# Kernel tuning notes

Measured on AMD Instinct MI355X. Metric: run time of the kernel, lower is better.

## Reference

```python
import jax, jax.numpy as jnp
import numpy as np

B, T, C, H = 4, 2048, 1024, 16
D = C // H  # head dim 64


def setup_inputs() -> dict:
    key = jax.random.key(0)
    ks = jax.random.split(key, 5)
    s = 1.0 / np.sqrt(C)
    return {
        "x": jax.random.normal(ks[0], (B, T, C), jnp.float32),
        "Wq": jax.random.normal(ks[1], (C, C), jnp.float32) * s,
        "bq": jnp.zeros((C,), jnp.float32),
        "Wk": jax.random.normal(ks[2], (C, C), jnp.float32) * s,
        "bk": jnp.zeros((C,), jnp.float32),
        "Wv": jax.random.normal(ks[3], (C, C), jnp.float32) * s,
        "bv": jnp.zeros((C,), jnp.float32),
        "Wp": jax.random.normal(ks[4], (C, C), jnp.float32) * s,
        "bp": jnp.zeros((C,), jnp.float32),
    }


def reference(x, Wq, bq, Wk, bk, Wv, bv, Wp, bp):
    # project and split heads: [B,T,C] -> [B,H,T,D]
    def heads(w, b):
        return (x @ w.T + b).reshape(B, T, H, D).transpose(0, 2, 1, 3)

    q = heads(Wq, bq)
    k = heads(Wk, bk)
    v = heads(Wv, bv)

    att = jnp.einsum("bhqd,bhkd->bhqk", q, k) * (1.0 / np.sqrt(D))
    causal = jnp.tril(jnp.ones((T, T), bool))  # [T,T]
    att = jnp.where(causal[None, None], att, -jnp.inf)
    att = jax.nn.softmax(att, axis=-1)
    # dropout prob is 0.0 -> identity
    y = jnp.einsum("bhqk,bhkd->bhqd", att, v)
    y = y.transpose(0, 2, 1, 3).reshape(B, T, C)
    return y @ Wp.T + bp
```

## Files before the change

### kernel.cpp

```cpp
#include <hip/hip_runtime.h>
#include <hip/hip_bf16.h>

#define BB 4
#define TT 2048
#define CC 1024
#define HH 16
#define DD 64
#define PSTR 72

typedef unsigned short u16;
typedef __attribute__((ext_vector_type(8))) short bf16x8;
typedef __attribute__((ext_vector_type(4))) float f32x4;
typedef __attribute__((ext_vector_type(16))) float f32x16;

__device__ __forceinline__ float bf2f(u16 v) {
    union { unsigned u; float f; } c; c.u = ((unsigned)v) << 16; return c.f;
}
__device__ __forceinline__ u16 f2bf(float f) {
    union { float f; unsigned u; } c; c.f = f;
    unsigned u = c.u + 0x7fffu + ((c.u >> 16) & 1u);
    return (u16)(u >> 16);
}
__device__ __forceinline__ float fast_exp2(float x) {
    float r;
    asm volatile("v_exp_f32 %0, %1\n\ts_nop 1" : "=v"(r) : "v"(x));
    return r;
}
__device__ __forceinline__ unsigned pack_bf16(unsigned b0, unsigned b1) {
    unsigned d;
    asm("v_perm_b32 %0, %1, %2, %3" : "=v"(d) : "v"(b1), "v"(b0), "v"(0x07060302u));
    return d;
}
__device__ __forceinline__ uint2 pack4(float v0, float v1, float v2, float v3) {
    uint2 pk;
    pk.x = pack_bf16(__float_as_uint(v0) + 0x8000u, __float_as_uint(v1) + 0x8000u);
    pk.y = pack_bf16(__float_as_uint(v2) + 0x8000u, __float_as_uint(v3) + 0x8000u);
    return pk;
}
__device__ __forceinline__ unsigned cvtpk_bf16(float lo, float hi) {
    unsigned r;
    asm("v_cvt_pk_bf16_f32 %0, %1, %2" : "=v"(r) : "v"(lo), "v"(hi));
    return r;
}
__device__ __forceinline__ void gload16(const u16* g, u16* l) {
    __builtin_amdgcn_global_load_lds(
        (const __attribute__((address_space(1))) void*)g,
        (__attribute__((address_space(3))) void*)l, 16, 0, 0);
}

__device__ __forceinline__ int detect_bf16(const u16* __restrict__ xprobe, int* sh) {
    const int t = threadIdx.x;
    u16 hh = xprobe[2 * t];
    int e = (hh >> 7) & 0xFF;
    unsigned long long m = __ballot(e >= 118 && e <= 132);
    if ((t & 63) == 0) sh[t >> 6] = __popcll(m);
    __syncthreads();
    return (sh[0] + sh[1] + sh[2] + sh[3]) >= 128;
}

struct CastArgs {
    const void* src[9];
    u16* dst[9];
    int blk_start[10];
    int n[9];
};
__global__ __launch_bounds__(256) void cast_all(CastArgs a, const u16* __restrict__ xprobe) {
    __shared__ int sh[4];
    const int isbf = detect_bf16(xprobe, sh);
    int b = blockIdx.x;
    int s = 0;
    while (s < 8 && b >= a.blk_start[s + 1]) s++;
    int i0 = (b - a.blk_start[s]) * 2048 + threadIdx.x * 8;
    if (i0 + 8 > a.n[s]) return;
    if (isbf) {
        *(uint4*)&a.dst[s][i0] = *(const uint4*)&((const u16*)a.src[s])[i0];
    } else {
        const float* sp = (const float*)a.src[s];
        u16 tmp[8];
#pragma unroll
        for (int j = 0; j < 8; j++) tmp[j] = f2bf(sp[i0 + j]);
        *(uint4*)&a.dst[s][i0] = *(uint4*)tmp;
    }
}

__device__ __forceinline__ void gemm_core(
    const u16* __restrict__ X, const u16* __restrict__ W,
    u16* Als, u16* Bls, f32x16 (&acc)[2][2],
    int m0, int n0, int wave, int lane, int wm, int wn)
{
    const int l32 = lane & 31;
    const int hv  = lane >> 5;
    int srow[4], sch[4];
#pragma unroll
    for (int c = 0; c < 4; c++) {
        srow[c] = wave * 32 + c * 8 + (lane >> 3);
        sch[c]  = (lane & 7) ^ (srow[c] & 7);
    }

    for (int k0 = 0; k0 < CC; k0 += 64) {
        __syncthreads();
#pragma unroll
        for (int c = 0; c < 4; c++) {
            gload16(&X[(size_t)(m0 + srow[c]) * CC + k0 + sch[c] * 8],
                    &Als[wave * 2048 + c * 512]);
            gload16(&W[(size_t)(n0 + srow[c]) * CC + k0 + sch[c] * 8],
                    &Bls[wave * 2048 + c * 512]);
        }
        __syncthreads();

#pragma unroll
        for (int ks = 0; ks < 4; ks++) {
            const int sw = ((ks * 2 + hv) ^ (l32 & 7)) * 8;
            bf16x8 a[2], b[2];
#pragma unroll
            for (int i = 0; i < 2; i++)
                a[i] = *(const bf16x8*)&Als[(wm + i * 32 + l32) * 64 + sw];
#pragma unroll
            for (int j = 0; j < 2; j++)
                b[j] = *(const bf16x8*)&Bls[(wn + j * 32 + l32) * 64 + sw];
#pragma unroll
            for (int i = 0; i < 2; i++)
#pragma unroll
                for (int j = 0; j < 2; j++)
                    acc[i][j] = __builtin_amdgcn_mfma_f32_32x32x16_bf16(
                        b[j], a[i], acc[i][j], 0, 0, 0);
        }
    }
}

__global__ __launch_bounds__(256, 2) void gemm_qkv(
    const u16* __restrict__ X,
    const u16* __restrict__ Wq, const u16* __restrict__ Wk, const u16* __restrict__ Wv,
    const u16* __restrict__ bq, const u16* __restrict__ bk, const u16* __restrict__ bv,
    u16* __restrict__ Q, u16* __restrict__ K, u16* __restrict__ VT)
{
    __shared__ __align__(16) u16 Als[128 * 64];
    __shared__ __align__(16) u16 Bls[3 * 128 * 64];

    const int tid  = threadIdx.x;
    const int wave = tid >> 6;
    const int lane = tid & 63;
    const int l32  = lane & 31;
    const int hv   = lane >> 5;
    const int m0   = blockIdx.x * 128;
    const int n0   = blockIdx.y * 128;
    const int wm   = (wave >> 1) * 64;
    const int wn   = (wave & 1) * 64;

    const u16* Ws[3]  = {Wq, Wk, Wv};

    f32x16 acc[3][2][2];
#pragma unroll
    for (int z = 0; z < 3; z++)
#pragma unroll
        for (int i = 0; i < 2; i++)
#pragma unroll
            for (int j = 0; j < 2; j++) acc[z][i][j] = (f32x16)0.0f;

    int srow[4], sch[4];
#pragma unroll
    for (int c = 0; c < 4; c++) {
        srow[c] = wave * 32 + c * 8 + (lane >> 3);
        sch[c]  = (lane & 7) ^ (srow[c] & 7);
    }

    for (int k0 = 0; k0 < CC; k0 += 64) {
        __syncthreads();
#pragma unroll
        for (int c = 0; c < 4; c++)
            gload16(&X[(size_t)(m0 + srow[c]) * CC + k0 + sch[c] * 8],
                    &Als[wave * 2048 + c * 512]);
#pragma unroll
        for (int z = 0; z < 3; z++)
#pragma unroll
            for (int c = 0; c < 4; c++)
                gload16(&Ws[z][(size_t)(n0 + srow[c]) * CC + k0 + sch[c] * 8],
                        &Bls[z * 8192 + wave * 2048 + c * 512]);
        __syncthreads();

#pragma unroll
        for (int ks = 0; ks < 4; ks++) {
            const int sw = ((ks * 2 + hv) ^ (l32 & 7)) * 8;
            bf16x8 a[2];
#pragma unroll
            for (int i = 0; i < 2; i++)
                a[i] = *(const bf16x8*)&Als[(wm + i * 32 + l32) * 64 + sw];
#pragma unroll
            for (int z = 0; z < 3; z++) {
                bf16x8 b[2];
#pragma unroll
                for (int j = 0; j < 2; j++)
                    b[j] = *(const bf16x8*)&Bls[z * 8192 + (wn + j * 32 + l32) * 64 + sw];
#pragma unroll
                for (int i = 0; i < 2; i++)
#pragma unroll
                    for (int j = 0; j < 2; j++)
                        acc[z][i][j] = __builtin_amdgcn_mfma_f32_32x32x16_bf16(
                            b[j], a[i], acc[z][i][j], 0, 0, 0);
            }
        }
    }

    const u16* biases[3] = {bq, bk, bv};
    u16* outs[3]         = {Q, K, VT};

#pragma unroll
    for (int z = 0; z < 3; z++) {
        const float scale = (z == 0) ? 0.18033688f : 1.0f;
        const u16* bias = biases[z];
        u16* outp = outs[z];
#pragma unroll
        for (int j = 0; j < 2; j++) {
#pragma unroll
            for (int rq = 0; rq < 4; rq++) {
                const int n_base = n0 + wn + j * 32 + rq * 8 + hv * 4;
                union { uint2 u; u16 us[4]; } braw;
                braw.u = *(const uint2*)&bias[n_base];
                const int hh = n_base >> 6, d0 = n_base & 63;
#pragma unroll
                for (int i = 0; i < 2; i++) {
                    const int m = m0 + wm + i * 32 + l32;
                    const int bb = m >> 11, t = m & (TT - 1);
                    float v0 = (acc[z][i][j][rq * 4 + 0] + bf2f(braw.us[0])) * scale;
                    float v1 = (acc[z][i][j][rq * 4 + 1] + bf2f(braw.us[1])) * scale;
                    float v2 = (acc[z][i][j][rq * 4 + 2] + bf2f(braw.us[2])) * scale;
                    float v3 = (acc[z][i][j][rq * 4 + 3] + bf2f(braw.us[3])) * scale;
                    if (z < 2) {
                        *(uint2*)&outp[((size_t)(bb * HH + hh) * TT + t) * DD + d0] =
                            pack4(v0, v1, v2, v3);
                    } else {
                        const size_t base = (size_t)(bb * HH + hh) * DD * TT + t;
                        outp[base + (size_t)(d0 + 0) * TT] = f2bf(v0);
                        outp[base + (size_t)(d0 + 1) * TT] = f2bf(v1);
                        outp[base + (size_t)(d0 + 2) * TT] = f2bf(v2);
                        outp[base + (size_t)(d0 + 3) * TT] = f2bf(v3);
                    }
                }
            }
        }
    }
}

__global__ __launch_bounds__(256, 4) void gemm_proj(
    const u16* __restrict__ X, const u16* __restrict__ W,
    const u16* __restrict__ bias, void* __restrict__ out,
    const u16* __restrict__ xprobe)
{
    __shared__ __align__(16) u16 Als[128 * 64];
    __shared__ __align__(16) u16 Bls[128 * 64];
    __shared__ int sh[4];

    const int isbf = detect_bf16(xprobe, sh);

    const int tid  = threadIdx.x;
    const int wave = tid >> 6;
    const int lane = tid & 63;
    const int l32  = lane & 31;
    const int hv   = lane >> 5;
    const int m0   = blockIdx.x * 128;
    const int n0   = blockIdx.y * 128;
    const int wm   = (wave >> 1) * 64;
    const int wn   = (wave & 1) * 64;

    f32x16 acc[2][2];
#pragma unroll
    for (int i = 0; i < 2; i++)
#pragma unroll
        for (int j = 0; j < 2; j++) acc[i][j] = (f32x16)0.0f;

    gemm_core(X, W, Als, Bls, acc, m0, n0, wave, lane, wm, wn);

#pragma unroll
    for (int j = 0; j < 2; j++) {
#pragma unroll
        for (int rq = 0; rq < 4; rq++) {
            const int n_base = n0 + wn + j * 32 + rq * 8 + hv * 4;
            union { uint2 u; u16 us[4]; } braw;
            braw.u = *(const uint2*)&bias[n_base];
#pragma unroll
            for (int i = 0; i < 2; i++) {
                const int m = m0 + wm + i * 32 + l32;
                float v0 = acc[i][j][rq * 4 + 0] + bf2f(braw.us[0]);
                float v1 = acc[i][j][rq * 4 + 1] + bf2f(braw.us[1]);
                float v2 = acc[i][j][rq * 4 + 2] + bf2f(braw.us[2]);
                float v3 = acc[i][j][rq * 4 + 3] + bf2f(braw.us[3]);
                if (isbf) {
                    *(uint2*)&((u16*)out)[(size_t)m * CC + n_base] = pack4(v0, v1, v2, v3);
                } else {
                    float4 f; f.x = v0; f.y = v1; f.z = v2; f.w = v3;
                    *(float4*)&((float*)out)[(size_t)m * CC + n_base] = f;
                }
            }
        }
    }
}

__global__ __launch_bounds__(256, 3) void attn_kernel(
    const u16* __restrict__ Qg, const u16* __restrict__ Kg,
    const u16* __restrict__ VTg, u16* __restrict__ Yg)
{
    __shared__ __align__(16) u16 Ks[2][64 * 64];
    __shared__ __align__(16) u16 VTs[2][64 * 64];
    __shared__ __align__(16) u16 Ps[128 * PSTR];
    __shared__ float ls[128];

    const int tid  = threadIdx.x;
    const int wave = tid >> 6;
    const int lane = tid & 63;
    const int quad = lane >> 4;
    const int l16  = lane & 15;
    const int ly   = (l16 & 7) ^ (l16 >> 3);
    const int bh    = blockIdx.x;
    const int qtile = (TT / 128 - 1) - blockIdx.y;
    const int h = bh & (HH - 1);
    const int b = bh >> 4;
    const int q0 = qtile * 128;

    bf16x8 qf[2][2];
#pragma unroll
    for (int g = 0; g < 2; g++)
#pragma unroll
        for (int ks = 0; ks < 2; ks++)
            qf[g][ks] = *(const bf16x8*)&Qg[((size_t)bh * TT + q0 + wave * 32 +
                                             g * 16 + l16) * DD + ks * 32 + quad * 8];

    const u16* kp[2];
    const u16* vp[2];
#pragma unroll
    for (int c = 0; c < 2; c++) {
        const int srow = wave * 16 + c * 8 + (lane >> 3);
        const int sch  = (lane & 7) ^ (lane >> 3) ^ ((wave * 2 + c) & 7);
        kp[c] = Kg + (size_t)bh * TT * DD + (size_t)srow * DD + sch * 8;
        vp[c] = VTg + (size_t)bh * DD * TT + (size_t)srow * TT + sch * 8;
    }

    f32x4 o_acc[2][4];
#pragma unroll
    for (int g = 0; g < 2; g++)
#pragma unroll
        for (int jt = 0; jt < 4; jt++) o_acc[g][jt] = (f32x4)0.0f;
    float lsum[2] = {0.0f, 0.0f};

    const int ntiles = 2 * qtile;
    const int nkv    = ntiles + 2;

#pragma unroll
    for (int c = 0; c < 2; c++) {
        gload16(kp[c], &Ks[0][wave * 1024 + c * 512]);
        gload16(vp[c], &VTs[0][wave * 1024 + c * 512]);
        kp[c] += 64 * DD;
        vp[c] += 64;
    }

    for (int kv = 0; kv < nkv; kv++) {
        const bool masked = (kv >= ntiles);
        const int cur = kv & 1;
        __syncthreads();
        if (kv + 1 < nkv) {
#pragma unroll
            for (int c = 0; c < 2; c++) {
                gload16(kp[c], &Ks[cur ^ 1][wave * 1024 + c * 512]);
                gload16(vp[c], &VTs[cur ^ 1][wave * 1024 + c * 512]);
                kp[c] += 64 * DD;
                vp[c] += 64;
            }
        }

        f32x4 st[2][4];
#pragma unroll
        for (int g = 0; g < 2; g++)
#pragma unroll
            for (int j = 0; j < 4; j++) st[g][j] = (f32x4)0.0f;
#pragma unroll
        for (int ks = 0; ks < 2; ks++) {
            const int rsw = ((ks * 4 + quad) ^ ly) * 8;
#pragma unroll
            for (int j = 0; j < 4; j++) {
                bf16x8 kf = *(const bf16x8*)&Ks[cur][(j * 16 + l16) * 64 + (rsw ^ (j * 16))];
#pragma unroll
                for (int g = 0; g < 2; g++)
                    st[g][j] = __builtin_amdgcn_mfma_f32_16x16x32_bf16(
                        kf, qf[g][ks], st[g][j], 0, 0, 0);
            }
        }

#pragma unroll
        for (int g = 0; g < 2; g++) {
            u16* psrow = &Ps[(wave * 32 + g * 16 + l16) * PSTR];
            const int qrow = q0 + wave * 32 + g * 16 + l16;
            float lp = 0.0f;
#pragma unroll
            for (int j = 0; j < 4; j++) {
                float e0 = fast_exp2(st[g][j][0]);
                float e1 = fast_exp2(st[g][j][1]);
                float e2 = fast_exp2(st[g][j][2]);
                float e3 = fast_exp2(st[g][j][3]);
                if (masked) {
                    const int kc = kv * 64 + j * 16 + quad * 4;
                    if (kc + 0 > qrow) e0 = 0.0f;
                    if (kc + 1 > qrow) e1 = 0.0f;
                    if (kc + 2 > qrow) e2 = 0.0f;
                    if (kc + 3 > qrow) e3 = 0.0f;
                }
                lp += (e0 + e1) + (e2 + e3);
                uint2 pk;
                pk.x = cvtpk_bf16(e0, e1);
                pk.y = cvtpk_bf16(e2, e3);
                *(uint2*)&psrow[j * 16 + quad * 4] = pk;
            }
            lsum[g] += lp;
        }

#pragma unroll
        for (int ks = 0; ks < 2; ks++) {
            const int rsw = ((ks * 4 + quad) ^ ly) * 8;
            bf16x8 vfk[4];
#pragma unroll
            for (int jt = 0; jt < 4; jt++)
                vfk[jt] = *(const bf16x8*)&VTs[cur][(jt * 16 + l16) * 64 + (rsw ^ (jt * 16))];
#pragma unroll
            for (int g = 0; g < 2; g++) {
                bf16x8 pf = *(const bf16x8*)&Ps[(wave * 32 + g * 16 + l16) * PSTR +
                                                ks * 32 + quad * 8];
#pragma unroll
                for (int jt = 0; jt < 4; jt++)
                    o_acc[g][jt] = __builtin_amdgcn_mfma_f32_16x16x32_bf16(
                        pf, vfk[jt], o_acc[g][jt], 0, 0, 0);
            }
        }
    }

#pragma unroll
    for (int g = 0; g < 2; g++) {
        lsum[g] += __shfl_xor(lsum[g], 16, 64);
        lsum[g] += __shfl_xor(lsum[g], 32, 64);
        ls[wave * 32 + g * 16 + l16] = lsum[g];
    }

#pragma unroll
    for (int g = 0; g < 2; g++) {
        float linv[4];
#pragma unroll
        for (int r = 0; r < 4; r++)
            linv[r] = 1.0f / fmaxf(ls[wave * 32 + g * 16 + quad * 4 + r], 1e-20f);
#pragma unroll
        for (int jt = 0; jt < 4; jt++) {
#pragma unroll
            for (int r = 0; r < 4; r++) {
                const int t = q0 + wave * 32 + g * 16 + quad * 4 + r;
                const int c = h * DD + jt * 16 + l16;
                Yg[((size_t)b * TT + t) * CC + c] = f2bf(o_acc[g][jt][r] * linv[r]);
            }
        }
    }
}

extern "C" void kernel_launch(void* const* d_in, const int* in_sizes, int n_in,
                              void* d_out, int out_size, void* d_ws, size_t ws_size,
                              hipStream_t stream) {
    u16* w = (u16*)d_ws;
    size_t off = 0;
    const size_t NX = (size_t)BB * TT * CC;
    const size_t NW = (size_t)CC * CC;
    const size_t NB = CC;
    const size_t per = (size_t)BB * HH * TT * DD;

    u16* xb  = w + off; off += NX;
    u16* Wqb = w + off; off += NW;
    u16* Wkb = w + off; off += NW;
    u16* Wvb = w + off; off += NW;
    u16* Wpb = w + off; off += NW;
    u16* bqb = w + off; off += NB;
    u16* bkb = w + off; off += NB;
    u16* bvb = w + off; off += NB;
    u16* bpb = w + off; off += NB;
    u16* Q   = w + off; off += per;
    u16* K   = w + off; off += per;
    u16* VT  = w + off; off += per;
    u16* Y   = w + off; off += per;

    CastArgs ca;
    const int srcmap[9] = {0, 1, 3, 5, 7, 2, 4, 6, 8};
    u16* dsts[9] = {xb, Wqb, Wkb, Wvb, Wpb, bqb, bkb, bvb, bpb};
    int ns[9] = {(int)NX, (int)NW, (int)NW, (int)NW, (int)NW,
                 (int)NB, (int)NB, (int)NB, (int)NB};
    int acc_blk = 0;
    for (int i = 0; i < 9; i++) {
        ca.src[i] = d_in[srcmap[i]];
        ca.dst[i] = dsts[i];
        ca.n[i]   = ns[i];
        ca.blk_start[i] = acc_blk;
        acc_blk += (ns[i] + 2047) / 2048;
    }
    ca.blk_start[9] = acc_blk;
    cast_all<<<acc_blk, 256, 0, stream>>>(ca, (const u16*)d_in[0]);

    gemm_qkv<<<dim3(64, 8), 256, 0, stream>>>(xb, Wqb, Wkb, Wvb,
                                              bqb, bkb, bvb, Q, K, VT);
    attn_kernel<<<dim3(BB * HH, TT / 128), 256, 0, stream>>>(Q, K, VT, Y);
    gemm_proj<<<dim3(64, 8), 256, 0, stream>>>(Y, Wpb, bpb, d_out,
                                               (const u16*)d_in[0]);
}
```

Measured before the change: 243.4 us.

## Double-buffer QKV GEMM shared-memory tiles with half-depth K steps

The fused QKV projection GEMM now uses two shared-memory buffers, each with a K-depth of 32 instead of one buffer of depth 64. The next K tile's global-to-LDS loads are issued right after a single barrier, so they overlap the MFMA work on the current tile. This replaces the load, sync, compute, sync pattern, and the row and chunk swizzle is adjusted for the narrower rows. In exchange there are twice as many K iterations, each carrying less MFMA work between barriers. Only the QKV GEMM changes; the attention and output-projection kernels are untouched.

```diff
diff --git a/kernel.cpp b/kernel.cpp
--- a/kernel.cpp
+++ b/kernel.cpp
@@ -134,8 +134,8 @@
     const u16* __restrict__ bq, const u16* __restrict__ bk, const u16* __restrict__ bv,
     u16* __restrict__ Q, u16* __restrict__ K, u16* __restrict__ VT)
 {
-    __shared__ __align__(16) u16 Als[128 * 64];
-    __shared__ __align__(16) u16 Bls[3 * 128 * 64];
+    __shared__ __align__(16) u16 Als[2][128 * 32];
+    __shared__ __align__(16) u16 Bls[2][3 * 128 * 32];
 
     const int tid  = threadIdx.x;
     const int wave = tid >> 6;
@@ -147,7 +147,7 @@
     const int wm   = (wave >> 1) * 64;
     const int wn   = (wave & 1) * 64;
 
-    const u16* Ws[3]  = {Wq, Wk, Wv};
+    const u16* Ws[3] = {Wq, Wk, Wv};
 
     f32x16 acc[3][2][2];
 #pragma unroll
@@ -157,40 +157,53 @@
 #pragma unroll
             for (int j = 0; j < 2; j++) acc[z][i][j] = (f32x16)0.0f;
 
-    int srow[4], sch[4];
-#pragma unroll
-    for (int c = 0; c < 4; c++) {
-        srow[c] = wave * 32 + c * 8 + (lane >> 3);
-        sch[c]  = (lane & 7) ^ (srow[c] & 7);
-    }
-
-    for (int k0 = 0; k0 < CC; k0 += 64) {
+    const int rloc = lane >> 2;
+    const int cchk = (lane & 3) ^ (rloc & 3);
+    int arow[2];
+#pragma unroll
+    for (int j = 0; j < 2; j++) arow[j] = wave * 32 + j * 16 + rloc;
+
+#pragma unroll
+    for (int j = 0; j < 2; j++)
+        gload16(&X[(size_t)(m0 + arow[j]) * CC + cchk * 8],
+                &Als[0][(wave * 128 + j * 64) * 8]);
+#pragma unroll
+    for (int z = 0; z < 3; z++)
+#pragma unroll
+        for (int j = 0; j < 2; j++)
+            gload16(&Ws[z][(size_t)(n0 + arow[j]) * CC + cchk * 8],
+                    &Bls[0][z * 4096 + (wave * 128 + j * 64) * 8]);
+
+    for (int t = 0; t < 32; ++t) {
+        const int cur = t & 1;
         __syncthreads();
-#pragma unroll
-        for (int c = 0; c < 4; c++)
-            gload16(&X[(size_t)(m0 + srow[c]) * CC + k0 + sch[c] * 8],
-                    &Als[wave * 2048 + c * 512]);
-#pragma unroll
-        for (int z = 0; z < 3; z++)
-#pragma unroll
-            for (int c = 0; c < 4; c++)
-                gload16(&Ws[z][(size_t)(n0 + srow[c]) * CC + k0 + sch[c] * 8],
-                        &Bls[z * 8192 + wave * 2048 + c * 512]);
-        __syncthreads();
-
-#pragma unroll
-        for (int ks = 0; ks < 4; ks++) {
-            const int sw = ((ks * 2 + hv) ^ (l32 & 7)) * 8;
+        if (t + 1 < 32) {
+            const int k1 = (t + 1) * 32;
+#pragma unroll
+            for (int j = 0; j < 2; j++)
+                gload16(&X[(size_t)(m0 + arow[j]) * CC + k1 + cchk * 8],
+                        &Als[cur ^ 1][(wave * 128 + j * 64) * 8]);
+#pragma unroll
+            for (int z = 0; z < 3; z++)
+#pragma unroll
+                for (int j = 0; j < 2; j++)
+                    gload16(&Ws[z][(size_t)(n0 + arow[j]) * CC + k1 + cchk * 8],
+                            &Bls[cur ^ 1][z * 4096 + (wave * 128 + j * 64) * 8]);
+        }
+
+#pragma unroll
+        for (int ks = 0; ks < 2; ks++) {
+            const int sw = ((ks * 2 + hv) ^ (l32 & 3)) * 8;
             bf16x8 a[2];
 #pragma unroll
             for (int i = 0; i < 2; i++)
-                a[i] = *(const bf16x8*)&Als[(wm + i * 32 + l32) * 64 + sw];
+                a[i] = *(const bf16x8*)&Als[cur][(wm + i * 32 + l32) * 32 + sw];
 #pragma unroll
             for (int z = 0; z < 3; z++) {
                 bf16x8 b[2];
 #pragma unroll
                 for (int j = 0; j < 2; j++)
-                    b[j] = *(const bf16x8*)&Bls[z * 8192 + (wn + j * 32 + l32) * 64 + sw];
+                    b[j] = *(const bf16x8*)&Bls[cur][z * 4096 + (wn + j * 32 + l32) * 32 + sw];
 #pragma unroll
                 for (int i = 0; i < 2; i++)
 #pragma unroll
```

After: 249.4 us. 2.5% more time.
